# Optimization experiments

Measured on AMD Instinct MI355X. Metric: run time of the kernel, lower is better.

## Reference

```python
import jax, jax.numpy as jnp
import numpy as np

S = 8192        # seq_length
H2 = 1024       # 2 * lstm_hidden_size
A = 2048        # attention_hidden_size
E = 768         # embedding_dim == pos_embedding_dim


def _bahdanau_weights(sentence, length, ctx, W_s, b_s, W_c, b_c, v, b_v):
    # sentence: [1, S, H2], ctx: [1, E_ctx]
    u = jnp.einsum('bsh,ha->bsa', sentence, W_s) + b_s \
        + (ctx @ W_c + b_c)[:, None, :]                    # [1, S, A]
    e = jnp.einsum('bsa,a->bs', jnp.tanh(u), v) + b_v       # [1, S]
    mask = jnp.arange(S)[None, :] >= length[:, None]        # [1, S] key mask
    e = jnp.where(mask, -jnp.inf, e)
    all_inf = jnp.all(mask, axis=1)                         # [1]
    # guard fully-masked rows so softmax stays finite, then zero them (matches torch)
    e_safe = jnp.where(all_inf[:, None], jnp.zeros_like(e), e)
    w = jax.nn.softmax(e_safe, axis=1)
    return jnp.where(all_inf[:, None], 0.0, w)              # [1, S]


def setup_inputs() -> dict:
    key = jax.random.key(0)
    ks = jax.random.split(key, 24)
    f = jax.random.normal
    sc_s = 1.0 / np.sqrt(H2)
    sc_c = 1.0 / np.sqrt(E)
    sc_v = 1.0 / np.sqrt(A)
    inp = {
        'sentence': f(ks[0], (1, S, H2), jnp.float32),
        'length': jax.random.randint(ks[1], (1,), 0, S),
        'pos_embedding': f(ks[2], (1, E), jnp.float32),
        'cardinal_phrase_embedding': f(ks[3], (1, E), jnp.float32),
        'headline_embedding': f(ks[4], (1, E), jnp.float32),
    }
    i = 5
    for tag in ('p', 'c', 'h'):
        inp[f'W_sent_{tag}'] = f(ks[i], (H2, A), jnp.float32) * sc_s; i += 1
        inp[f'b_sent_{tag}'] = f(ks[i], (A,), jnp.float32) * sc_s; i += 1
        inp[f'W_ctx_{tag}'] = f(ks[i], (E, A), jnp.float32) * sc_c; i += 1
        inp[f'b_ctx_{tag}'] = f(ks[i], (A,), jnp.float32) * sc_c; i += 1
        inp[f'v_{tag}'] = f(ks[i], (A,), jnp.float32) * sc_v; i += 1
        inp[f'bv_{tag}'] = f(ks[i], (), jnp.float32) * sc_v; i += 1
    return inp


def reference(sentence, length, pos_embedding, cardinal_phrase_embedding,
              headline_embedding,
              W_sent_p, b_sent_p, W_ctx_p, b_ctx_p, v_p, bv_p,
              W_sent_c, b_sent_c, W_ctx_c, b_ctx_c, v_c, bv_c,
              W_sent_h, b_sent_h, W_ctx_h, b_ctx_h, v_h, bv_h):
    w_pos = _bahdanau_weights(sentence, length, pos_embedding,
                              W_sent_p, b_sent_p, W_ctx_p, b_ctx_p, v_p, bv_p)
    w_card = _bahdanau_weights(sentence, length, cardinal_phrase_embedding,
                               W_sent_c, b_sent_c, W_ctx_c, b_ctx_c, v_c, bv_c)
    w_head = _bahdanau_weights(sentence, length, headline_embedding,
                               W_sent_h, b_sent_h, W_ctx_h, b_ctx_h, v_h, bv_h)
    fused = (w_pos + w_card + w_head) / 3.0                 # [1, S]
    return jnp.einsum('bs,bsh->bh', fused, sentence)        # [1, H2]
```

## Files before the change

### kernel.cpp

```cpp
#include <hip/hip_runtime.h>
#include <hip/hip_bf16.h>
#include <stdint.h>


namespace {

constexpr int S = 8192;
constexpr int H = 1024;
constexpr int A = 2048;
constexpr int E = 768;

typedef __bf16 bf16x8 __attribute__((ext_vector_type(8)));
typedef float f32x4 __attribute__((ext_vector_type(4)));

__device__ __forceinline__ bf16x8 cvt8(float4 lo, float4 hi) {
  bf16x8 r;
  r[0] = (__bf16)lo.x; r[1] = (__bf16)lo.y; r[2] = (__bf16)lo.z; r[3] = (__bf16)lo.w;
  r[4] = (__bf16)hi.x; r[5] = (__bf16)hi.y; r[6] = (__bf16)hi.z; r[7] = (__bf16)hi.w;
  return r;
}

__global__ __launch_bounds__(256)
void k_prep(const float* __restrict__ sentence, __bf16* __restrict__ packA,
            const float* __restrict__ Wp, const float* __restrict__ Wc_s,
            const float* __restrict__ Wh, __bf16* __restrict__ packB,
            const float* __restrict__ ctx_p, const float* __restrict__ ctx_c,
            const float* __restrict__ ctx_h,
            const float* __restrict__ Wcx_p, const float* __restrict__ Wcx_c,
            const float* __restrict__ Wcx_h,
            const float* __restrict__ bs_p, const float* __restrict__ bs_c,
            const float* __restrict__ bs_h,
            const float* __restrict__ bc_p, const float* __restrict__ bc_c,
            const float* __restrict__ bc_h,
            float* __restrict__ ctxb_q, float* __restrict__ e_arr,
            const int* __restrict__ length, float* __restrict__ out, int n_out) {
  __shared__ float tile[64][65];
  int b = blockIdx.x;
  int t = threadIdx.x;

  if (b < 4096) {
    int len = min(max(length[0], 0), S);
    int lenp = (len + 63) & ~63;
    if ((b >> 4) * 32 >= lenp) return;
    int C = b * 256 + t;
    int seg = C >> 6;
    int g = seg >> 6, kt = (seg >> 1) & 31, f = seg & 1;
    int slot = C & 63, quad = slot >> 4, l16 = slot & 15;
    const float4* s4 =
        (const float4*)(sentence + (size_t)(g * 32 + f * 16 + l16) * H + kt * 32 + quad * 8);
    *(bf16x8*)(packA + (size_t)seg * 512 + slot * 8) = cvt8(s4[0], s4[1]);
  } else if (b < 5632) {
    int r = b - 4096;
    int head = r >> 9; r &= 511;
    const float* W = head == 0 ? Wp : (head == 1 ? Wc_s : Wh);
    int a0 = (r & 31) * 64;
    int k0 = (r >> 5) * 64;
#pragma unroll
    for (int i = 0; i < 8; ++i) {
      int idx = t + i * 256;
      int rr = idx >> 5;
      int cc = (idx & 31) * 2;
      float2 w2 = *(const float2*)&W[(size_t)(k0 + rr) * A + a0 + cc];
      tile[cc][rr] = w2.x;
      tile[cc + 1][rr] = w2.y;
    }
    __syncthreads();
#pragma unroll
    for (int i = 0; i < 2; ++i) {
      int c = t + i * 256;
      int segl = c >> 6;
      int cgl = segl >> 1, ktl = segl & 1;
      int slot = c & 63, quad = slot >> 4, l16 = slot & 15;
      int al = cgl * 16 + l16;
      int kl = ktl * 32 + quad * 8;
      bf16x8 o;
#pragma unroll
      for (int e = 0; e < 8; ++e) o[e] = (__bf16)tile[al][kl + e];
      size_t seg = ((size_t)head * 128 + (a0 >> 4) + cgl) * 32 + (k0 >> 5) + ktl;
      *(bf16x8*)(packB + seg * 512 + slot * 8) = o;
    }
  } else if (b < 5728) {
    int r = b - 5632;
    int head = r >> 5;
    int sub = r & 31;
    int ablk = sub & 7;
    int eq = sub >> 3;
    const float* ctx = head == 0 ? ctx_p : (head == 1 ? ctx_c : ctx_h);
    const float* Wc  = head == 0 ? Wcx_p : (head == 1 ? Wcx_c : Wcx_h);
    int a = ablk * 256 + t;
    float s = 0.f;
    if (eq == 0) {
      const float* bs = head == 0 ? bs_p : (head == 1 ? bs_c : bs_h);
      const float* bc = head == 0 ? bc_p : (head == 1 ? bc_c : bc_h);
      s = bs[a] + bc[a];
    }
    int e0 = eq * 192;
#pragma unroll 8
    for (int e = e0; e < e0 + 192; ++e) s = fmaf(ctx[e], Wc[(size_t)e * A + a], s);
    ctxb_q[eq * 3 * A + head * A + a] = s;
  } else {
    int idx = (b - 5728) * 256 + t;
    float4 z = {0.f, 0.f, 0.f, 0.f};
    int total = 6144 + (n_out >> 2);
    for (int i = idx; i < total; i += 2048) {
      if (i < 6144) ((float4*)e_arr)[i] = z;
      else ((float4*)out)[i - 6144] = z;
    }
  }
}

__global__ __launch_bounds__(256)
void k_gemm_e(const __bf16* __restrict__ packA, const __bf16* __restrict__ packB,
              const float* __restrict__ ctxb_q,
              const float* __restrict__ v_p, const float* __restrict__ v_c,
              const float* __restrict__ v_h,
              const int* __restrict__ length, float* __restrict__ e_out) {
  int bid = blockIdx.x;
  int xcd = bid & 7;
  int j = bid >> 3;
  int mt = j / 6;
  int pl = j - mt * 6;
  int panel = xcd * 6 + pl;
  int n0 = (panel & 15) * 128;
  int head = panel >> 4;

  int m0 = mt * 64;
  int len = min(max(length[0], 0), S);
  if (m0 >= len) return;
  const float* v  = head == 0 ? v_p : (head == 1 ? v_c : v_h);
  float* e_h = e_out + head * S;

  __shared__ float e_part[64];

  int tid = threadIdx.x;
  if (tid < 64) e_part[tid] = 0.f;
  __syncthreads();

  int lane = tid & 63;
  int wave = tid >> 6;
  int wm = wave >> 1, wn = wave & 1;
  int quad = lane >> 4, l16 = lane & 15;

  f32x4 acc[2][4];
#pragma unroll
  for (int i = 0; i < 2; ++i)
#pragma unroll
    for (int j2 = 0; j2 < 4; ++j2) acc[i][j2] = (f32x4){0.f, 0.f, 0.f, 0.f};

  const __bf16* gA = packA + ((size_t)(m0 >> 5) + wm) * 64 * 512 + (size_t)lane * 8;
  const __bf16* gB =
      packB + (((size_t)head * 128 + (n0 >> 4) + wn * 4) * 32) * 512 + (size_t)lane * 8;

  bf16x8 xa0, xa1, ya0, ya1;
  bf16x8 xb0, xb1, xb2, xb3, yb0, yb1, yb2, yb3;

#define LOADA(sl, kt)                                   \
  do {                                                  \
    sl##0 = *(const bf16x8*)(gA + ((kt) << 10));        \
    sl##1 = *(const bf16x8*)(gA + ((kt) << 10) + 512);  \
  } while (0)

#define LOADB(sl, kt)                                        \
  do {                                                       \
    sl##0 = *(const bf16x8*)(gB + ((size_t)(kt) << 9));          \
    sl##1 = *(const bf16x8*)(gB + ((size_t)(32 + (kt)) << 9));   \
    sl##2 = *(const bf16x8*)(gB + ((size_t)(64 + (kt)) << 9));   \
    sl##3 = *(const bf16x8*)(gB + ((size_t)(96 + (kt)) << 9));   \
  } while (0)

#define COMPUTE(asl, bsl)                                                                     \
  do {                                                                                        \
    acc[0][0] = __builtin_amdgcn_mfma_f32_16x16x32_bf16(asl##0, bsl##0, acc[0][0], 0, 0, 0);  \
    acc[1][0] = __builtin_amdgcn_mfma_f32_16x16x32_bf16(asl##1, bsl##0, acc[1][0], 0, 0, 0);  \
    acc[0][1] = __builtin_amdgcn_mfma_f32_16x16x32_bf16(asl##0, bsl##1, acc[0][1], 0, 0, 0);  \
    acc[1][1] = __builtin_amdgcn_mfma_f32_16x16x32_bf16(asl##1, bsl##1, acc[1][1], 0, 0, 0);  \
    acc[0][2] = __builtin_amdgcn_mfma_f32_16x16x32_bf16(asl##0, bsl##2, acc[0][2], 0, 0, 0);  \
    acc[1][2] = __builtin_amdgcn_mfma_f32_16x16x32_bf16(asl##1, bsl##2, acc[1][2], 0, 0, 0);  \
    acc[0][3] = __builtin_amdgcn_mfma_f32_16x16x32_bf16(asl##0, bsl##3, acc[0][3], 0, 0, 0);  \
    acc[1][3] = __builtin_amdgcn_mfma_f32_16x16x32_bf16(asl##1, bsl##3, acc[1][3], 0, 0, 0);  \
  } while (0)

  LOADA(xa, 0);
  LOADB(xb, 0);
#pragma unroll 1
  for (int kt = 0; kt < 30; kt += 2) {
    LOADA(ya, kt + 1);
    LOADB(yb, kt + 1);
    COMPUTE(xa, xb);
    LOADA(xa, kt + 2);
    LOADB(xb, kt + 2);
    COMPUTE(ya, yb);
  }
  LOADA(ya, 31);
  LOADB(yb, 31);
  COMPUTE(xa, xb);
  COMPUTE(ya, yb);

#undef LOADA
#undef LOADB
#undef COMPUTE

  float vj[4], cbj[4];
#pragma unroll
  for (int j2 = 0; j2 < 4; ++j2) {
    int col = n0 + wn * 64 + j2 * 16 + l16;
    vj[j2] = v[col];
    cbj[j2] = ctxb_q[head * A + col] + ctxb_q[3 * A + head * A + col] +
              ctxb_q[6 * A + head * A + col] + ctxb_q[9 * A + head * A + col];
  }
#pragma unroll
  for (int i = 0; i < 2; ++i) {
#pragma unroll
    for (int r = 0; r < 4; ++r) {
      float p = 0.f;
#pragma unroll
      for (int j2 = 0; j2 < 4; ++j2) {
        float u = acc[i][j2][r] + cbj[j2];
        float ex = __expf(2.f * u);
        float th = 1.f - 2.f / (ex + 1.f);
        p = fmaf(th, vj[j2], p);
      }
      p += __shfl_xor(p, 1);
      p += __shfl_xor(p, 2);
      p += __shfl_xor(p, 4);
      p += __shfl_xor(p, 8);
      if (l16 == 0) atomicAdd(&e_part[wm * 32 + i * 16 + quad * 4 + r], p);
    }
  }
  __syncthreads();
  if (tid < 64) atomicAdd(&e_h[m0 + tid], e_part[tid]);
}

__global__ void k_out(const float* __restrict__ sent, const float* __restrict__ e_arr,
                      const int* __restrict__ length, float* __restrict__ out) {
  int len = min(max(length[0], 0), S);
  int r0 = blockIdx.x * 16;
  if (r0 >= len) return;
  int tid = threadIdx.x;

  __shared__ float red[3][4];
  __shared__ float sstat[6];
  __shared__ float wrow[16];

#pragma unroll
  for (int h = 0; h < 3; ++h) {
    const float* e_h = e_arr + h * S;
    float m = -3.4e38f;
    for (int s = tid; s < len; s += 256) m = fmaxf(m, e_h[s]);
#pragma unroll
    for (int o = 32; o >= 1; o >>= 1) m = fmaxf(m, __shfl_xor(m, o));
    if ((tid & 63) == 0) red[h][tid >> 6] = m;
  }
  __syncthreads();
  if (tid < 3) sstat[tid * 2] = fmaxf(fmaxf(red[tid][0], red[tid][1]),
                                      fmaxf(red[tid][2], red[tid][3]));
  __syncthreads();
#pragma unroll
  for (int h = 0; h < 3; ++h) {
    const float* e_h = e_arr + h * S;
    float mm = sstat[h * 2];
    float ss = 0.f;
    for (int s = tid; s < len; s += 256) ss += __expf(e_h[s] - mm);
#pragma unroll
    for (int o = 32; o >= 1; o >>= 1) ss += __shfl_xor(ss, o);
    if ((tid & 63) == 0) red[h][tid >> 6] = ss;
  }
  __syncthreads();
  if (tid < 3) sstat[tid * 2 + 1] = red[tid][0] + red[tid][1] + red[tid][2] + red[tid][3];
  __syncthreads();

  if (tid < 16 && r0 + tid < len) {
    int r = r0 + tid;
    wrow[tid] = (__expf(e_arr[r] - sstat[0]) / sstat[1] +
                 __expf(e_arr[S + r] - sstat[2]) / sstat[3] +
                 __expf(e_arr[2 * S + r] - sstat[4]) / sstat[5]) * (1.f / 3.f);
  }
  __syncthreads();

  int col = tid * 4;
  int rend = min(r0 + 16, len);
  float4 acc = {0.f, 0.f, 0.f, 0.f};
  for (int r = r0; r < rend; ++r) {
    float w = wrow[r - r0];
    float4 x = *(const float4*)(sent + (size_t)r * H + col);
    acc.x = fmaf(w, x.x, acc.x);
    acc.y = fmaf(w, x.y, acc.y);
    acc.z = fmaf(w, x.z, acc.z);
    acc.w = fmaf(w, x.w, acc.w);
  }
  atomicAdd(&out[col + 0], acc.x);
  atomicAdd(&out[col + 1], acc.y);
  atomicAdd(&out[col + 2], acc.z);
  atomicAdd(&out[col + 3], acc.w);
}

}

extern "C" void kernel_launch(void* const* d_in, const int* in_sizes, int n_in,
                              void* d_out, int out_size, void* d_ws, size_t ws_size,
                              hipStream_t stream) {
  const float* sentence = (const float*)d_in[0];
  const int* length     = (const int*)d_in[1];
  const float* ctx_p = (const float*)d_in[2];
  const float* ctx_c = (const float*)d_in[3];
  const float* ctx_h = (const float*)d_in[4];
  const float* W_s[3] = {(const float*)d_in[5],  (const float*)d_in[11], (const float*)d_in[17]};
  const float* b_s[3] = {(const float*)d_in[6],  (const float*)d_in[12], (const float*)d_in[18]};
  const float* W_c[3] = {(const float*)d_in[7],  (const float*)d_in[13], (const float*)d_in[19]};
  const float* b_c[3] = {(const float*)d_in[8],  (const float*)d_in[14], (const float*)d_in[20]};
  const float* v_[3]  = {(const float*)d_in[9],  (const float*)d_in[15], (const float*)d_in[21]};
  float* out = (float*)d_out;

  char* ws = (char*)d_ws;
  __bf16* packA  = (__bf16*)(ws);
  __bf16* packB  = (__bf16*)(ws + 16777216);
  float* ctxb_q  = (float*)(ws + 29360128);
  float* e_arr   = (float*)(ws + 29458432);

  k_prep<<<5736, 256, 0, stream>>>(sentence, packA,
                                   W_s[0], W_s[1], W_s[2], packB,
                                   ctx_p, ctx_c, ctx_h,
                                   W_c[0], W_c[1], W_c[2],
                                   b_s[0], b_s[1], b_s[2],
                                   b_c[0], b_c[1], b_c[2], ctxb_q, e_arr,
                                   length, out, out_size);
  k_gemm_e<<<6144, 256, 0, stream>>>(packA, packB, ctxb_q,
                                     v_[0], v_[1], v_[2], length, e_arr);
  k_out<<<S / 16, 256, 0, stream>>>(sentence, e_arr, length, out);
}
```

Baseline: 213.7 us.

## Double GEMM M-tile to 128 rows and coalesce sentence packing reads

Each k_gemm_e block now covers 128 rows instead of 64, with each wave holding 4x4 MFMA accumulators. Every B fragment is reused across twice as many A fragments, and the grid is halved. The prep kernel now maps threads row-major over the sentence so fp32 global reads are contiguous, scattering the bf16 writes into the packed layout instead. The cost is more registers per thread, which may lower occupancy, and length masking now works at 128-row granularity, so some padded rows get computed.

```diff
diff --git a/kernel.cpp b/kernel.cpp
--- a/kernel.cpp
+++ b/kernel.cpp
@@ -40,15 +40,16 @@
 
   if (b < 4096) {
     int len = min(max(length[0], 0), S);
-    int lenp = (len + 63) & ~63;
-    if ((b >> 4) * 32 >= lenp) return;
+    int lenp = (len + 127) & ~127;
+    if (b * 2 >= lenp) return;
     int C = b * 256 + t;
-    int seg = C >> 6;
-    int g = seg >> 6, kt = (seg >> 1) & 31, f = seg & 1;
-    int slot = C & 63, quad = slot >> 4, l16 = slot & 15;
-    const float4* s4 =
-        (const float4*)(sentence + (size_t)(g * 32 + f * 16 + l16) * H + kt * 32 + quad * 8);
-    *(bf16x8*)(packA + (size_t)seg * 512 + slot * 8) = cvt8(s4[0], s4[1]);
+    int row = C >> 7;
+    int k8 = C & 127;
+    const float4* s4 = (const float4*)(sentence + (size_t)row * H + k8 * 8);
+    int g = row >> 5, f = (row >> 4) & 1, l16 = row & 15;
+    int kt = k8 >> 2, quad = k8 & 3;
+    size_t dst = ((size_t)(g * 64 + kt * 2 + f)) * 512 + (quad * 16 + l16) * 8;
+    *(bf16x8*)(packA + dst) = cvt8(s4[0], s4[1]);
   } else if (b < 5632) {
     int r = b - 4096;
     int head = r >> 9; r &= 511;
@@ -124,16 +125,16 @@
   int n0 = (panel & 15) * 128;
   int head = panel >> 4;
 
-  int m0 = mt * 64;
+  int m0 = mt * 128;
   int len = min(max(length[0], 0), S);
   if (m0 >= len) return;
   const float* v  = head == 0 ? v_p : (head == 1 ? v_c : v_h);
   float* e_h = e_out + head * S;
 
-  __shared__ float e_part[64];
+  __shared__ float e_part[128];
 
   int tid = threadIdx.x;
-  if (tid < 64) e_part[tid] = 0.f;
+  if (tid < 128) e_part[tid] = 0.f;
   __syncthreads();
 
   int lane = tid & 63;
@@ -141,27 +142,29 @@
   int wm = wave >> 1, wn = wave & 1;
   int quad = lane >> 4, l16 = lane & 15;
 
-  f32x4 acc[2][4];
-#pragma unroll
-  for (int i = 0; i < 2; ++i)
+  f32x4 acc[4][4];
+#pragma unroll
+  for (int i = 0; i < 4; ++i)
 #pragma unroll
     for (int j2 = 0; j2 < 4; ++j2) acc[i][j2] = (f32x4){0.f, 0.f, 0.f, 0.f};
 
-  const __bf16* gA = packA + ((size_t)(m0 >> 5) + wm) * 64 * 512 + (size_t)lane * 8;
+  const __bf16* gA = packA + ((size_t)(m0 >> 5) + wm * 2) * 64 * 512 + (size_t)lane * 8;
   const __bf16* gB =
       packB + (((size_t)head * 128 + (n0 >> 4) + wn * 4) * 32) * 512 + (size_t)lane * 8;
 
-  bf16x8 xa0, xa1, ya0, ya1;
+  bf16x8 xa0, xa1, xa2, xa3, ya0, ya1, ya2, ya3;
   bf16x8 xb0, xb1, xb2, xb3, yb0, yb1, yb2, yb3;
 
-#define LOADA(sl, kt)                                   \
-  do {                                                  \
-    sl##0 = *(const bf16x8*)(gA + ((kt) << 10));        \
-    sl##1 = *(const bf16x8*)(gA + ((kt) << 10) + 512);  \
+#define LOADA(sl, kt)                                                \
+  do {                                                               \
+    sl##0 = *(const bf16x8*)(gA + ((size_t)((kt)*2 + 0) << 9));      \
+    sl##1 = *(const bf16x8*)(gA + ((size_t)((kt)*2 + 1) << 9));      \
+    sl##2 = *(const bf16x8*)(gA + ((size_t)(64 + (kt)*2 + 0) << 9)); \
+    sl##3 = *(const bf16x8*)(gA + ((size_t)(64 + (kt)*2 + 1) << 9)); \
   } while (0)
 
-#define LOADB(sl, kt)                                        \
-  do {                                                       \
+#define LOADB(sl, kt)                                            \
+  do {                                                           \
     sl##0 = *(const bf16x8*)(gB + ((size_t)(kt) << 9));          \
     sl##1 = *(const bf16x8*)(gB + ((size_t)(32 + (kt)) << 9));   \
     sl##2 = *(const bf16x8*)(gB + ((size_t)(64 + (kt)) << 9));   \
@@ -170,14 +173,14 @@
 
 #define COMPUTE(asl, bsl)                                                                     \
   do {                                                                                        \
-    acc[0][0] = __builtin_amdgcn_mfma_f32_16x16x32_bf16(asl##0, bsl##0, acc[0][0], 0, 0, 0);  \
-    acc[1][0] = __builtin_amdgcn_mfma_f32_16x16x32_bf16(asl##1, bsl##0, acc[1][0], 0, 0, 0);  \
-    acc[0][1] = __builtin_amdgcn_mfma_f32_16x16x32_bf16(asl##0, bsl##1, acc[0][1], 0, 0, 0);  \
-    acc[1][1] = __builtin_amdgcn_mfma_f32_16x16x32_bf16(asl##1, bsl##1, acc[1][1], 0, 0, 0);  \
-    acc[0][2] = __builtin_amdgcn_mfma_f32_16x16x32_bf16(asl##0, bsl##2, acc[0][2], 0, 0, 0);  \
-    acc[1][2] = __builtin_amdgcn_mfma_f32_16x16x32_bf16(asl##1, bsl##2, acc[1][2], 0, 0, 0);  \
-    acc[0][3] = __builtin_amdgcn_mfma_f32_16x16x32_bf16(asl##0, bsl##3, acc[0][3], 0, 0, 0);  \
-    acc[1][3] = __builtin_amdgcn_mfma_f32_16x16x32_bf16(asl##1, bsl##3, acc[1][3], 0, 0, 0);  \
+    _Pragma("unroll")                                                                         \
+    for (int jj = 0; jj < 4; ++jj) {                                                          \
+      bf16x8 bf_ = jj == 0 ? bsl##0 : (jj == 1 ? bsl##1 : (jj == 2 ? bsl##2 : bsl##3));       \
+      acc[0][jj] = __builtin_amdgcn_mfma_f32_16x16x32_bf16(asl##0, bf_, acc[0][jj], 0, 0, 0); \
+      acc[1][jj] = __builtin_amdgcn_mfma_f32_16x16x32_bf16(asl##1, bf_, acc[1][jj], 0, 0, 0); \
+      acc[2][jj] = __builtin_amdgcn_mfma_f32_16x16x32_bf16(asl##2, bf_, acc[2][jj], 0, 0, 0); \
+      acc[3][jj] = __builtin_amdgcn_mfma_f32_16x16x32_bf16(asl##3, bf_, acc[3][jj], 0, 0, 0); \
+    }                                                                                         \
   } while (0)
 
   LOADA(xa, 0);
@@ -209,7 +212,7 @@
               ctxb_q[6 * A + head * A + col] + ctxb_q[9 * A + head * A + col];
   }
 #pragma unroll
-  for (int i = 0; i < 2; ++i) {
+  for (int i = 0; i < 4; ++i) {
 #pragma unroll
     for (int r = 0; r < 4; ++r) {
       float p = 0.f;
@@ -224,11 +227,11 @@
       p += __shfl_xor(p, 2);
       p += __shfl_xor(p, 4);
       p += __shfl_xor(p, 8);
-      if (l16 == 0) atomicAdd(&e_part[wm * 32 + i * 16 + quad * 4 + r], p);
-    }
-  }
-  __syncthreads();
-  if (tid < 64) atomicAdd(&e_h[m0 + tid], e_part[tid]);
+      if (l16 == 0) atomicAdd(&e_part[wm * 64 + i * 16 + quad * 4 + r], p);
+    }
+  }
+  __syncthreads();
+  if (tid < 128) atomicAdd(&e_h[m0 + tid], e_part[tid]);
 }
 
 __global__ void k_out(const float* __restrict__ sent, const float* __restrict__ e_arr,
@@ -324,7 +327,7 @@
                                    b_s[0], b_s[1], b_s[2],
                                    b_c[0], b_c[1], b_c[2], ctxb_q, e_arr,
                                    length, out, out_size);
-  k_gemm_e<<<6144, 256, 0, stream>>>(packA, packB, ctxb_q,
+  k_gemm_e<<<3072, 256, 0, stream>>>(packA, packB, ctxb_q,
                                      v_[0], v_[1], v_[2], length, e_arr);
   k_out<<<S / 16, 256, 0, stream>>>(sentence, e_arr, length, out);
 }
```

New measurement: 205.9 us. 3.7% less time.
